# Kernel optimization log

Measured on AMD Instinct MI355X. Metric: run time of the kernel, lower is better.

The kernel has to match this reference:

```python
import jax, jax.numpy as jnp
import numpy as np

NX, NY, NZ = 432, 496, 1   # grid_size (nx, ny, nz), nz must be 1
NBEV = 128                 # NUM_BEV_FEATURES
K = 4                      # NUM_K
SHRINK = 0.0025            # SHRINK_TH
BN_EPS = 1e-3


def setup_inputs():
    key = jax.random.key(0)
    ks = jax.random.split(key, 8)
    B, P, NPT, D, M = 2, 6000, 4096, 64, 1024
    pillar_features = jax.random.normal(ks[0], (B, P, D), jnp.float32)
    point_features = jax.random.normal(ks[1], (B, NPT, D), jnp.float32)
    # unique flat BEV cells per scene -> coords columns (z, y, x) as in OpenPCDet coords[:,1:4]
    coords = []
    for b in range(B):
        flat = jax.random.permutation(jax.random.fold_in(ks[2], b), NX * NY)[:P]
        y = flat // NX
        x = flat % NX
        z = jnp.zeros_like(flat)
        coords.append(jnp.stack([z, y, x], axis=1))
    voxel_coords = jnp.stack(coords, 0).astype(jnp.int32)
    adapt_w = jax.random.normal(ks[3], (NBEV // 2, D * K), jnp.float32) * 0.05  # Linear(no bias)
    mem_w = jax.random.normal(ks[4], (M, D), jnp.float32) * 0.05               # MemoryUnit slots
    bn_gamma = jnp.ones((NBEV // 2,), jnp.float32)
    bn_beta = jnp.zeros((NBEV // 2,), jnp.float32)
    return dict(pillar_features=pillar_features, point_features=point_features,
                voxel_coords=voxel_coords, adapt_w=adapt_w, mem_w=mem_w,
                bn_gamma=bn_gamma, bn_beta=bn_beta)


def _forward(pillar_features, point_features, voxel_coords, adapt_w, mem_w, bn_gamma, bn_beta):
    def per_batch(pillars, points, coords):
        # pillars [P,D], points [Np,D], coords [P,3] = (z, y, x)
        # get_score: softmax over points dim, top-k points per pillar
        score = jax.nn.softmax(pillars @ points.T, axis=1)            # [P,Np]
        _, idx = jax.lax.top_k(score, K)                              # [P,K] (indices detached)
        pts = points[idx]                                             # [P,K,D]
        # MemoryUnit (MemAE-style): softmax attention over memory, hard-shrink-relu, L1 renorm
        x = pts.reshape(-1, points.shape[1])                          # [P*K,D]
        att = jax.nn.softmax(x @ mem_w.T, axis=1)                     # [P*K,M]
        shr = jax.nn.relu(att - SHRINK) * att / (jnp.abs(att - SHRINK) + 1e-12)
        att = shr / (jnp.sum(jnp.abs(shr), axis=1, keepdims=True) + 1e-12)
        mem_out = (att @ mem_w).reshape(pillars.shape[0], -1)         # [P, K*D]
        # adapt_layer (Linear, no bias) -> BatchNorm1d (training stats over pillars) -> ReLU
        h = mem_out @ adapt_w.T                                       # [P, NBEV//2]
        mu = jnp.mean(h, axis=0)
        var = jnp.var(h, axis=0)
        h = (h - mu) / jnp.sqrt(var + BN_EPS) * bn_gamma + bn_beta
        h = jax.nn.relu(h)
        feats = jnp.concatenate([pillars, h], axis=1)                 # [P, NBEV]
        # scatter into dense BEV grid: index = z + y*nx + x (nz==1 so z==0)
        flat = coords[:, 0] + coords[:, 1] * NX + coords[:, 2]
        spatial = jnp.zeros((NBEV, NZ * NX * NY), feats.dtype).at[:, flat].set(feats.T)
        pind = jnp.zeros((3, NZ * NX * NY), feats.dtype)
        pind = pind.at[0, flat].set(coords[:, 1].astype(feats.dtype))
        pind = pind.at[1, flat].set(coords[:, 2].astype(feats.dtype))
        pind = pind.at[2, flat].set(coords[:, 0].astype(feats.dtype))
        return spatial, pind

    spatial, pind = jax.vmap(per_batch)(pillar_features, point_features, voxel_coords)
    B = spatial.shape[0]
    return spatial.reshape(B, NBEV * NZ, NY, NX), pind.reshape(B, 3 * NZ, NY, NX)


def reference(pillar_features, point_features, voxel_coords, adapt_w, mem_w, bn_gamma, bn_beta):
    return _forward(pillar_features, point_features, voxel_coords, adapt_w, mem_w, bn_gamma, bn_beta)
```

## Files before the change

### kernel.cpp

```cpp
#include <hip/hip_runtime.h>

#define NXg 432
#define NYg 496
#define SCELLS (NXg*NYg)
#define PB 6000
#define NPTS 4096
#define DD 64
#define MM 1024
#define KK 4
#define BB 2
#define NROWS (PB*KK)
#define NSEG 16
#define SEGPTS (NPTS/NSEG)
#define CHROWS 64
#define NCHNK (SEGPTS/CHROWS)
#define AR 32
#define SHRINK_TH 0.0025f
#define BN_EPS 1e-3f
#define NEG_INF -3.402823466e38f

#define INS4(v, id, v0,v1,v2,v3, i0,i1,i2,i3) { \
    bool g0 = (v) > v0, g1 = (v) > v1, g2 = (v) > v2; \
    v3 = g2 ? v2 : (v);              i3 = g2 ? i2 : (id); \
    v2 = g2 ? (g1 ? v1 : (v)) : v2;  i2 = g2 ? (g1 ? i1 : (id)) : i2; \
    v1 = g1 ? (g0 ? v0 : (v)) : v1;  i1 = g1 ? (g0 ? i0 : (id)) : i1; \
    v0 = g0 ? (v) : v0;              i0 = g0 ? (id) : i0; \
}

__global__ __launch_bounds__(256) void k_init_inv(int* __restrict__ inv) {
    int i = blockIdx.x*256 + threadIdx.x;
    inv[i] = -1;
}

__global__ __launch_bounds__(256) void k_scatter_inv(const int* __restrict__ coords,
                                                     int* __restrict__ inv) {
    int i = blockIdx.x*256 + threadIdx.x;
    if (i >= BB*PB) return;
    int b = i / PB, p = i % PB;
    const int* c = coords + (size_t)i*3;
    int flat = c[0] + c[1]*NXg + c[2];
    inv[b*SCELLS + flat] = p;
}

__global__ __launch_bounds__(256) void k_score_topk(const float* __restrict__ pillars,
                                                    const float* __restrict__ points,
                                                    float* __restrict__ pV,
                                                    int* __restrict__ pI) {
    __shared__ float4 sPt[CHROWS*16];
    const int b = blockIdx.y;
    const int seg = blockIdx.z;
    const int t = threadIdx.x;
    const int pillar = blockIdx.x*256 + t;
    const int prow = pillar < PB ? pillar : PB-1;
    const int j0 = seg * SEGPTS;

    const float4* pil4  = (const float4*)pillars;
    const float4* ptsB4 = (const float4*)(points + (size_t)b*NPTS*DD);

    float4 wreg[16];
    #pragma unroll
    for (int d4 = 0; d4 < 16; d4++)
        wreg[d4] = pil4[((size_t)b*PB + prow)*16 + d4];

    float tv0=NEG_INF, tv1=NEG_INF, tv2=NEG_INF, tv3=NEG_INF;
    int   ti0=0, ti1=0, ti2=0, ti3=0;

    for (int ch = 0; ch < NCHNK; ch++) {
        const float4* src = ptsB4 + (size_t)(j0 + ch*CHROWS)*16;
        for (int i = t; i < CHROWS*16; i += 256)
            sPt[i] = src[i];
        __syncthreads();

        const int jb = j0 + ch*CHROWS;
        for (int j = 0; j < CHROWS; j += 2) {
            float a0 = 0.f, a1 = 0.f;
            #pragma unroll
            for (int d4 = 0; d4 < 16; d4++) {
                float4 x0 = sPt[j*16 + d4];
                float4 x1 = sPt[(j+1)*16 + d4];
                a0 += wreg[d4].x*x0.x + wreg[d4].y*x0.y + wreg[d4].z*x0.z + wreg[d4].w*x0.w;
                a1 += wreg[d4].x*x1.x + wreg[d4].y*x1.y + wreg[d4].z*x1.z + wreg[d4].w*x1.w;
            }
            if (a0 > tv3) INS4(a0, jb+j,   tv0,tv1,tv2,tv3, ti0,ti1,ti2,ti3)
            if (a1 > tv3) INS4(a1, jb+j+1, tv0,tv1,tv2,tv3, ti0,ti1,ti2,ti3)
        }
        __syncthreads();
    }

    if (pillar < PB) {
        size_t ob = (((size_t)b*NSEG + seg)*PB + pillar)*KK;
        pV[ob+0]=tv0; pV[ob+1]=tv1; pV[ob+2]=tv2; pV[ob+3]=tv3;
        pI[ob+0]=ti0; pI[ob+1]=ti1; pI[ob+2]=ti2; pI[ob+3]=ti3;
    }
}

__global__ __launch_bounds__(256) void k_merge(const float* __restrict__ pV,
                                               const int* __restrict__ pI,
                                               int* __restrict__ idxOut) {
    int i = blockIdx.x*256 + threadIdx.x;
    if (i >= BB*PB) return;
    int b = i / PB, p = i % PB;
    float fv0=NEG_INF, fv1=NEG_INF, fv2=NEG_INF, fv3=NEG_INF;
    int fi0=0, fi1=0, fi2=0, fi3=0;
    for (int s = 0; s < NSEG; s++) {
        size_t base = (((size_t)b*NSEG + s)*PB + p)*KK;
        #pragma unroll
        for (int q = 0; q < 4; q++) {
            float v = pV[base+q];
            if (v > fv3) INS4(v, pI[base+q], fv0,fv1,fv2,fv3, fi0,fi1,fi2,fi3)
        }
    }
    idxOut[(size_t)i*KK+0]=fi0; idxOut[(size_t)i*KK+1]=fi1;
    idxOut[(size_t)i*KK+2]=fi2; idxOut[(size_t)i*KK+3]=fi3;
}

__global__ __launch_bounds__(256) void k_logits(const float* __restrict__ points,
                                                const int* __restrict__ idxIn,
                                                const float* __restrict__ memw,
                                                float* __restrict__ logits,
                                                int b) {
    __shared__ float4 sX4[64*16];
    __shared__ int sId[64];
    const int t = threadIdx.x;
    const int lane = t & 63, wv = t >> 6;
    const int row0 = blockIdx.x * 64;
    const int cg = blockIdx.y * 256 + wv * 64;

    if (t < 64) sId[t] = idxIn[(size_t)b*NROWS + row0 + t];

    const float4* mw4 = (const float4*)memw;
    float4 wreg[16];
    #pragma unroll
    for (int d4 = 0; d4 < 16; d4++) wreg[d4] = mw4[(size_t)(cg + lane)*16 + d4];

    __syncthreads();
    const float4* ptsB4 = (const float4*)(points + (size_t)b*NPTS*DD);
    for (int i = t; i < 1024; i += 256) {
        int r = i >> 4, c = i & 15;
        sX4[i] = ptsB4[(size_t)sId[r]*16 + c];
    }
    __syncthreads();

    for (int r = 0; r < 64; r += 2) {
        float a0 = 0.f, a1 = 0.f;
        #pragma unroll
        for (int d4 = 0; d4 < 16; d4++) {
            float4 x0 = sX4[r*16 + d4];
            float4 x1 = sX4[(r+1)*16 + d4];
            a0 += wreg[d4].x*x0.x + wreg[d4].y*x0.y + wreg[d4].z*x0.z + wreg[d4].w*x0.w;
            a1 += wreg[d4].x*x1.x + wreg[d4].y*x1.y + wreg[d4].z*x1.z + wreg[d4].w*x1.w;
        }
        logits[(size_t)(row0 + r)*MM + cg + lane] = a0;
        logits[(size_t)(row0 + r + 1)*MM + cg + lane] = a1;
    }
}

__global__ __launch_bounds__(256) void k_stats(const float* __restrict__ logits,
                                               float* __restrict__ stats,
                                               int b) {
    const int wv = threadIdx.x >> 6, lane = threadIdx.x & 63;
    const int row = blockIdx.x*4 + wv;
    const float4* lg4 = (const float4*)logits;
    size_t base = (size_t)row*256;
    float4 l0 = lg4[base + lane];
    float4 l1 = lg4[base + 64 + lane];
    float4 l2 = lg4[base + 128 + lane];
    float4 l3 = lg4[base + 192 + lane];
    float m = fmaxf(fmaxf(fmaxf(l0.x,l0.y),fmaxf(l0.z,l0.w)),
             fmaxf(fmaxf(fmaxf(l1.x,l1.y),fmaxf(l1.z,l1.w)),
             fmaxf(fmaxf(fmaxf(l2.x,l2.y),fmaxf(l2.z,l2.w)),
                   fmaxf(fmaxf(l3.x,l3.y),fmaxf(l3.z,l3.w)))));
    #pragma unroll
    for (int off = 1; off < 64; off <<= 1) m = fmaxf(m, __shfl_xor(m, off));
    l0.x=__expf(l0.x-m); l0.y=__expf(l0.y-m); l0.z=__expf(l0.z-m); l0.w=__expf(l0.w-m);
    l1.x=__expf(l1.x-m); l1.y=__expf(l1.y-m); l1.z=__expf(l1.z-m); l1.w=__expf(l1.w-m);
    l2.x=__expf(l2.x-m); l2.y=__expf(l2.y-m); l2.z=__expf(l2.z-m); l2.w=__expf(l2.w-m);
    l3.x=__expf(l3.x-m); l3.y=__expf(l3.y-m); l3.z=__expf(l3.z-m); l3.w=__expf(l3.w-m);
    float s = (l0.x+l0.y+l0.z+l0.w) + (l1.x+l1.y+l1.z+l1.w)
            + (l2.x+l2.y+l2.z+l2.w) + (l3.x+l3.y+l3.z+l3.w);
    #pragma unroll
    for (int off = 1; off < 64; off <<= 1) s += __shfl_xor(s, off);
    float rinv = 1.f / s;
    float sh = 0.f;
    {
        float e, tt;
        e=l0.x*rinv; tt=e-SHRINK_TH; sh += tt>0.f ? e*tt/(tt+1e-12f) : 0.f;
        e=l0.y*rinv; tt=e-SHRINK_TH; sh += tt>0.f ? e*tt/(tt+1e-12f) : 0.f;
        e=l0.z*rinv; tt=e-SHRINK_TH; sh += tt>0.f ? e*tt/(tt+1e-12f) : 0.f;
        e=l0.w*rinv; tt=e-SHRINK_TH; sh += tt>0.f ? e*tt/(tt+1e-12f) : 0.f;
        e=l1.x*rinv; tt=e-SHRINK_TH; sh += tt>0.f ? e*tt/(tt+1e-12f) : 0.f;
        e=l1.y*rinv; tt=e-SHRINK_TH; sh += tt>0.f ? e*tt/(tt+1e-12f) : 0.f;
        e=l1.z*rinv; tt=e-SHRINK_TH; sh += tt>0.f ? e*tt/(tt+1e-12f) : 0.f;
        e=l1.w*rinv; tt=e-SHRINK_TH; sh += tt>0.f ? e*tt/(tt+1e-12f) : 0.f;
        e=l2.x*rinv; tt=e-SHRINK_TH; sh += tt>0.f ? e*tt/(tt+1e-12f) : 0.f;
        e=l2.y*rinv; tt=e-SHRINK_TH; sh += tt>0.f ? e*tt/(tt+1e-12f) : 0.f;
        e=l2.z*rinv; tt=e-SHRINK_TH; sh += tt>0.f ? e*tt/(tt+1e-12f) : 0.f;
        e=l2.w*rinv; tt=e-SHRINK_TH; sh += tt>0.f ? e*tt/(tt+1e-12f) : 0.f;
        e=l3.x*rinv; tt=e-SHRINK_TH; sh += tt>0.f ? e*tt/(tt+1e-12f) : 0.f;
        e=l3.y*rinv; tt=e-SHRINK_TH; sh += tt>0.f ? e*tt/(tt+1e-12f) : 0.f;
        e=l3.z*rinv; tt=e-SHRINK_TH; sh += tt>0.f ? e*tt/(tt+1e-12f) : 0.f;
        e=l3.w*rinv; tt=e-SHRINK_TH; sh += tt>0.f ? e*tt/(tt+1e-12f) : 0.f;
    }
    #pragma unroll
    for (int off = 1; off < 64; off <<= 1) sh += __shfl_xor(sh, off);
    if (lane == 0) {
        float4* st4 = (float4*)stats;
        st4[(size_t)b*NROWS + row] = make_float4(m, rinv, 1.f/(sh + 1e-12f), 0.f);
    }
}

__global__ __launch_bounds__(256) void k_attg(const float* __restrict__ logits,
                                              const float* __restrict__ memw,
                                              const float* __restrict__ stats,
                                              float* __restrict__ mo,
                                              int b) {
    __shared__ __align__(16) float sAtt[AR*68];
    __shared__ __align__(16) float4 sW4[64*16];
    __shared__ float sSt[AR*4];
    const int t = threadIdx.x;
    const int cg = t & 15, rg = t >> 4;
    const int row0 = blockIdx.x * AR;

    if (t < AR) {
        const float4* st4 = (const float4*)stats;
        float4 s = st4[(size_t)b*NROWS + row0 + t];
        sSt[t*4+0]=s.x; sSt[t*4+1]=s.y; sSt[t*4+2]=s.z; sSt[t*4+3]=s.w;
    }
    __syncthreads();

    const float4* lg4 = (const float4*)logits;
    const float4* mw4 = (const float4*)memw;
    float4 acc0 = make_float4(0.f,0.f,0.f,0.f);
    float4 acc1 = make_float4(0.f,0.f,0.f,0.f);

    for (int tile = 0; tile < 16; tile++) {
        #pragma unroll
        for (int q = 0; q < 2; q++) {
            int idx = q*256 + t;
            int row = idx >> 4, m4 = idx & 15;
            float4 lg = lg4[(size_t)(row0 + row)*256 + tile*16 + m4];
            float m = sSt[row*4], rinv = sSt[row*4+1], rsc = sSt[row*4+2];
            float4 o; float e, tt;
            e=__expf(lg.x-m)*rinv; tt=e-SHRINK_TH; o.x=(tt>0.f?e*tt/(tt+1e-12f):0.f)*rsc;
            e=__expf(lg.y-m)*rinv; tt=e-SHRINK_TH; o.y=(tt>0.f?e*tt/(tt+1e-12f):0.f)*rsc;
            e=__expf(lg.z-m)*rinv; tt=e-SHRINK_TH; o.z=(tt>0.f?e*tt/(tt+1e-12f):0.f)*rsc;
            e=__expf(lg.w-m)*rinv; tt=e-SHRINK_TH; o.w=(tt>0.f?e*tt/(tt+1e-12f):0.f)*rsc;
            *(float4*)(sAtt + row*68 + m4*4) = o;
        }
        #pragma unroll
        for (int q = 0; q < 4; q++) {
            int idx = q*256 + t;
            sW4[idx] = mw4[(size_t)tile*1024 + idx];
        }
        __syncthreads();
        #pragma unroll 4
        for (int m4 = 0; m4 < 16; m4++) {
            float4 a0 = *(const float4*)(sAtt + (rg*2+0)*68 + m4*4);
            float4 a1 = *(const float4*)(sAtt + (rg*2+1)*68 + m4*4);
            float4 w0 = sW4[(m4*4+0)*16 + cg];
            float4 w1 = sW4[(m4*4+1)*16 + cg];
            float4 w2 = sW4[(m4*4+2)*16 + cg];
            float4 w3 = sW4[(m4*4+3)*16 + cg];
            acc0.x += a0.x*w0.x + a0.y*w1.x + a0.z*w2.x + a0.w*w3.x;
            acc0.y += a0.x*w0.y + a0.y*w1.y + a0.z*w2.y + a0.w*w3.y;
            acc0.z += a0.x*w0.z + a0.y*w1.z + a0.z*w2.z + a0.w*w3.z;
            acc0.w += a0.x*w0.w + a0.y*w1.w + a0.z*w2.w + a0.w*w3.w;
            acc1.x += a1.x*w0.x + a1.y*w1.x + a1.z*w2.x + a1.w*w3.x;
            acc1.y += a1.x*w0.y + a1.y*w1.y + a1.z*w2.y + a1.w*w3.y;
            acc1.z += a1.x*w0.z + a1.y*w1.z + a1.z*w2.z + a1.w*w3.z;
            acc1.w += a1.x*w0.w + a1.y*w1.w + a1.z*w2.w + a1.w*w3.w;
        }
        __syncthreads();
    }

    *(float4*)(mo + (size_t)(row0 + rg*2 + 0)*64 + cg*4) = acc0;
    *(float4*)(mo + (size_t)(row0 + rg*2 + 1)*64 + cg*4) = acc1;
}

__global__ __launch_bounds__(256) void k_adapt(const float* __restrict__ mo,
                                               const float* __restrict__ adaptw,
                                               float* __restrict__ hOut,
                                               int b) {
    __shared__ float4 sMo4[12*64];
    const int t = threadIdx.x;
    const int lane = t & 63, wv = t >> 6;
    const int p0 = blockIdx.x * 12;

    const float4* mo4 = (const float4*)(mo + (size_t)p0*256);
    #pragma unroll
    for (int q = 0; q < 3; q++)
        sMo4[q*256 + t] = mo4[q*256 + t];
    __syncthreads();

    const float4* adG4 = (const float4*)adaptw;
    float h0 = 0.f, h1 = 0.f, h2 = 0.f;
    #pragma unroll
    for (int qt = 0; qt < 4; qt++) {
        float4 wreg[16];
        #pragma unroll
        for (int i = 0; i < 16; i++)
            wreg[i] = adG4[(size_t)lane*64 + qt*16 + i];
        #pragma unroll
        for (int i = 0; i < 16; i++) {
            float4 q0 = sMo4[(wv+0)*64 + qt*16 + i];
            float4 q1 = sMo4[(wv+4)*64 + qt*16 + i];
            float4 q2 = sMo4[(wv+8)*64 + qt*16 + i];
            h0 += wreg[i].x*q0.x + wreg[i].y*q0.y + wreg[i].z*q0.z + wreg[i].w*q0.w;
            h1 += wreg[i].x*q1.x + wreg[i].y*q1.y + wreg[i].z*q1.z + wreg[i].w*q1.w;
            h2 += wreg[i].x*q2.x + wreg[i].y*q2.y + wreg[i].z*q2.z + wreg[i].w*q2.w;
        }
    }
    hOut[((size_t)b*PB + p0 + wv + 0)*DD + lane] = h0;
    hOut[((size_t)b*PB + p0 + wv + 4)*DD + lane] = h1;
    hOut[((size_t)b*PB + p0 + wv + 8)*DD + lane] = h2;
}

__global__ __launch_bounds__(256) void k_bn1(const float* __restrict__ h,
                                             float* __restrict__ pSum,
                                             float* __restrict__ pSq) {
    const int bid = blockIdx.x;
    const int b = bid >> 5, ch = bid & 31;
    const int r0 = ch*188;
    int r1 = r0 + 188; if (r1 > PB) r1 = PB;
    __shared__ float sS[4*64], sS2[4*64];
    const int t = threadIdx.x;
    const int c = t & 63, stripe = t >> 6;
    float s = 0.f, s2 = 0.f;
    for (int r = r0 + stripe; r < r1; r += 4) {
        float v = h[((size_t)b*PB + r)*DD + c];
        s += v; s2 += v*v;
    }
    sS[stripe*64 + c] = s; sS2[stripe*64 + c] = s2;
    __syncthreads();
    if (t < 64) {
        float ts = sS[t] + sS[64+t] + sS[128+t] + sS[192+t];
        float ts2 = sS2[t] + sS2[64+t] + sS2[128+t] + sS2[192+t];
        pSum[(size_t)bid*64 + t] = ts;
        pSq[(size_t)bid*64 + t] = ts2;
    }
}

__global__ __launch_bounds__(64) void k_bn2(const float* __restrict__ pSum,
                                            const float* __restrict__ pSq,
                                            const float* __restrict__ gamma,
                                            float* __restrict__ bnMu,
                                            float* __restrict__ bnScale) {
    const int b = blockIdx.x;
    const int t = threadIdx.x;
    float ts = 0.f, ts2 = 0.f;
    for (int ch = 0; ch < 32; ch++) {
        ts += pSum[(size_t)(b*32 + ch)*64 + t];
        ts2 += pSq[(size_t)(b*32 + ch)*64 + t];
    }
    float mu = ts / (float)PB;
    float var = ts2 / (float)PB - mu*mu;
    if (var < 0.f) var = 0.f;
    bnMu[b*64+t] = mu;
    bnScale[b*64+t] = gamma[t] / sqrtf(var + BN_EPS);
}

__global__ __launch_bounds__(256) void k_fill(const int* __restrict__ inv,
                                              const float* __restrict__ pillars,
                                              const float* __restrict__ h,
                                              const float* __restrict__ bnMu,
                                              const float* __restrict__ bnScale,
                                              const float* __restrict__ beta,
                                              float* __restrict__ out) {
    const int b = blockIdx.y;
    const int f = blockIdx.x*256 + threadIdx.x;
    __shared__ float sMu[64], sSc[64], sBe[64];
    if (threadIdx.x < 64) {
        sMu[threadIdx.x] = bnMu[b*64+threadIdx.x];
        sSc[threadIdx.x] = bnScale[b*64+threadIdx.x];
        sBe[threadIdx.x] = beta[threadIdx.x];
    }
    __syncthreads();
    int iv = inv[b*SCELLS + f];
    bool occ = iv >= 0;
    int iv0 = occ ? iv : 0;
    float* sp = out + (size_t)b*128*SCELLS;
    const float* prow = pillars + ((size_t)b*PB + iv0)*DD;
    const float* hrow = h + ((size_t)b*PB + iv0)*DD;
    #pragma unroll 4
    for (int c = 0; c < 64; c++)
        sp[(size_t)c*SCELLS + f] = occ ? prow[c] : 0.f;
    #pragma unroll 4
    for (int c = 0; c < 64; c++) {
        float v = 0.f;
        if (occ) {
            float hv = hrow[c];
            v = fmaxf((hv - sMu[c])*sSc[c] + sBe[c], 0.f);
        }
        sp[(size_t)(64+c)*SCELLS + f] = v;
    }
    float* pi = out + (size_t)BB*128*SCELLS + (size_t)b*3*SCELLS;
    pi[f]              = occ ? (float)(f / NXg) : 0.f;
    pi[SCELLS + f]     = occ ? (float)(f % NXg) : 0.f;
    pi[2*(size_t)SCELLS + f] = 0.f;
}

extern "C" void kernel_launch(void* const* d_in, const int* in_sizes, int n_in,
                              void* d_out, int out_size, void* d_ws, size_t ws_size,
                              hipStream_t stream) {
    const float* pillars = (const float*)d_in[0];
    const float* points  = (const float*)d_in[1];
    const int*   coords  = (const int*)d_in[2];
    const float* adaptw  = (const float*)d_in[3];
    const float* memw    = (const float*)d_in[4];
    const float* gamma   = (const float*)d_in[5];
    const float* beta    = (const float*)d_in[6];
    float* out = (float*)d_out;

    char* w = (char*)d_ws;
    int* inv = (int*)w;        w += (size_t)BB*SCELLS*4;
    int* idx = (int*)w;        w += (size_t)BB*PB*KK*4;
    float* h = (float*)w;      w += (size_t)BB*PB*DD*4;
    float* bnMu = (float*)w;   w += (size_t)BB*64*4;
    float* bnScale = (float*)w; w += (size_t)BB*64*4;
    float* pSum = (float*)w;   w += (size_t)BB*32*64*4;
    float* pSq = (float*)w;    w += (size_t)BB*32*64*4;
    float* stats = (float*)w;  w += (size_t)BB*NROWS*4*4;
    float* mo = (float*)w;     w += (size_t)NROWS*DD*4;
    float* logits = (float*)w;
    float* pV = logits;
    int*   pI = (int*)(logits + (size_t)BB*NSEG*PB*KK);

    k_init_inv<<<dim3(BB*SCELLS/256), dim3(256), 0, stream>>>(inv);
    k_scatter_inv<<<dim3((BB*PB+255)/256), dim3(256), 0, stream>>>(coords, inv);
    k_score_topk<<<dim3((PB+255)/256, BB, NSEG), dim3(256), 0, stream>>>(pillars, points, pV, pI);
    k_merge<<<dim3((BB*PB+255)/256), dim3(256), 0, stream>>>(pV, pI, idx);
    for (int b = 0; b < BB; b++) {
        k_logits<<<dim3(NROWS/64, 4), dim3(256), 0, stream>>>(points, idx, memw, logits, b);
        k_stats<<<dim3(NROWS/4), dim3(256), 0, stream>>>(logits, stats, b);
        k_attg<<<dim3(NROWS/AR), dim3(256), 0, stream>>>(logits, memw, stats, mo, b);
        k_adapt<<<dim3(PB/12), dim3(256), 0, stream>>>(mo, adaptw, h, b);
    }
    k_bn1<<<dim3(BB*32), dim3(256), 0, stream>>>(h, pSum, pSq);
    k_bn2<<<dim3(BB), dim3(64), 0, stream>>>(pSum, pSq, gamma, bnMu, bnScale);
    k_fill<<<dim3(SCELLS/256, BB), dim3(256), 0, stream>>>(inv, pillars, h, bnMu, bnScale, beta, out);
}
```

Measured before the change: 627.4 us.

## Retile logits GEMM into 64x64 shared-memory tiles with 4x4 register blocking

```diff
diff --git a/kernel.cpp b/kernel.cpp
--- a/kernel.cpp
+++ b/kernel.cpp
@@ -15,6 +15,7 @@
 #define CHROWS 64
 #define NCHNK (SEGPTS/CHROWS)
 #define AR 32
+#define LRS 68
 #define SHRINK_TH 0.0025f
 #define BN_EPS 1e-3f
 #define NEG_INF -3.402823466e38f
@@ -119,40 +120,57 @@
                                                 const float* __restrict__ memw,
                                                 float* __restrict__ logits,
                                                 int b) {
-    __shared__ float4 sX4[64*16];
+    __shared__ float sX[64*LRS];
+    __shared__ float sW[64*LRS];
     __shared__ int sId[64];
     const int t = threadIdx.x;
-    const int lane = t & 63, wv = t >> 6;
+    const int cg = t & 15, rg = t >> 4;
     const int row0 = blockIdx.x * 64;
-    const int cg = blockIdx.y * 256 + wv * 64;
+    const int col0 = blockIdx.y * 64;
 
     if (t < 64) sId[t] = idxIn[(size_t)b*NROWS + row0 + t];
-
+    __syncthreads();
+
+    const float4* ptsB4 = (const float4*)(points + (size_t)b*NPTS*DD);
     const float4* mw4 = (const float4*)memw;
-    float4 wreg[16];
-    #pragma unroll
-    for (int d4 = 0; d4 < 16; d4++) wreg[d4] = mw4[(size_t)(cg + lane)*16 + d4];
-
-    __syncthreads();
-    const float4* ptsB4 = (const float4*)(points + (size_t)b*NPTS*DD);
-    for (int i = t; i < 1024; i += 256) {
-        int r = i >> 4, c = i & 15;
-        sX4[i] = ptsB4[(size_t)sId[r]*16 + c];
-    }
-    __syncthreads();
-
-    for (int r = 0; r < 64; r += 2) {
-        float a0 = 0.f, a1 = 0.f;
-        #pragma unroll
-        for (int d4 = 0; d4 < 16; d4++) {
-            float4 x0 = sX4[r*16 + d4];
-            float4 x1 = sX4[(r+1)*16 + d4];
-            a0 += wreg[d4].x*x0.x + wreg[d4].y*x0.y + wreg[d4].z*x0.z + wreg[d4].w*x0.w;
-            a1 += wreg[d4].x*x1.x + wreg[d4].y*x1.y + wreg[d4].z*x1.z + wreg[d4].w*x1.w;
-        }
-        logits[(size_t)(row0 + r)*MM + cg + lane] = a0;
-        logits[(size_t)(row0 + r + 1)*MM + cg + lane] = a1;
-    }
+    #pragma unroll
+    for (int q = 0; q < 4; q++) {
+        int idx = q*256 + t;
+        int r = idx >> 4, c4 = idx & 15;
+        *(float4*)(sX + r*LRS + c4*4) = ptsB4[(size_t)sId[r]*16 + c4];
+        float4 wv = mw4[(size_t)(col0 + r)*16 + c4];
+        sW[(c4*4+0)*LRS + r] = wv.x;
+        sW[(c4*4+1)*LRS + r] = wv.y;
+        sW[(c4*4+2)*LRS + r] = wv.z;
+        sW[(c4*4+3)*LRS + r] = wv.w;
+    }
+    __syncthreads();
+
+    float4 acc[4];
+    #pragma unroll
+    for (int i = 0; i < 4; i++) acc[i] = make_float4(0.f,0.f,0.f,0.f);
+
+    #pragma unroll
+    for (int k4 = 0; k4 < 16; k4++) {
+        float4 a[4], w[4];
+        #pragma unroll
+        for (int i = 0; i < 4; i++)
+            a[i] = *(const float4*)(sX + (rg*4+i)*LRS + k4*4);
+        #pragma unroll
+        for (int kk = 0; kk < 4; kk++)
+            w[kk] = *(const float4*)(sW + (k4*4+kk)*LRS + cg*4);
+        #pragma unroll
+        for (int i = 0; i < 4; i++) {
+            acc[i].x += a[i].x*w[0].x + a[i].y*w[1].x + a[i].z*w[2].x + a[i].w*w[3].x;
+            acc[i].y += a[i].x*w[0].y + a[i].y*w[1].y + a[i].z*w[2].y + a[i].w*w[3].y;
+            acc[i].z += a[i].x*w[0].z + a[i].y*w[1].z + a[i].z*w[2].z + a[i].w*w[3].z;
+            acc[i].w += a[i].x*w[0].w + a[i].y*w[1].w + a[i].z*w[2].w + a[i].w*w[3].w;
+        }
+    }
+
+    #pragma unroll
+    for (int i = 0; i < 4; i++)
+        *(float4*)(logits + (size_t)(row0 + rg*4 + i)*MM + col0 + cg*4) = acc[i];
 }
 
 __global__ __launch_bounds__(256) void k_stats(const float* __restrict__ logits,
@@ -430,7 +448,7 @@
     k_score_topk<<<dim3((PB+255)/256, BB, NSEG), dim3(256), 0, stream>>>(pillars, points, pV, pI);
     k_merge<<<dim3((BB*PB+255)/256), dim3(256), 0, stream>>>(pV, pI, idx);
     for (int b = 0; b < BB; b++) {
-        k_logits<<<dim3(NROWS/64, 4), dim3(256), 0, stream>>>(points, idx, memw, logits, b);
+        k_logits<<<dim3(NROWS/64, MM/64), dim3(256), 0, stream>>>(points, idx, memw, logits, b);
         k_stats<<<dim3(NROWS/4), dim3(256), 0, stream>>>(logits, stats, b);
         k_attg<<<dim3(NROWS/AR), dim3(256), 0, stream>>>(logits, memw, stats, mo, b);
         k_adapt<<<dim3(PB/12), dim3(256), 0, stream>>>(mo, adaptw, h, b);
```

Result: no change. 639.2 us (+1.9%).
